# Optimization experiments

Hardware: AMD Instinct MI355X
Metric: run time of the kernel (lower is better)

Reference implementation:

```python
import jax, jax.numpy as jnp
from jax import lax
import numpy as np

N_QUBITS = 10  # min(dim, n_wires) wires carry RX gates; rest stay |0>


def setup_inputs() -> dict:
    key = jax.random.key(0)
    k1, k2, k3, k4 = jax.random.split(key, 4)
    T, B, D, H, C = 128, 512, 512, 512, 32
    inputs = jax.random.normal(k1, (T, B, D), dtype=jnp.float32)
    # 4 gates (f, i, g, o), centres init ~ 0.1 * randn as in the module
    centres = 0.1 * jax.random.normal(k2, (4, C, D + H), dtype=jnp.float32)
    lin_w = jax.random.normal(k3, (4, H, C), dtype=jnp.float32) / jnp.sqrt(jnp.float32(C))
    lin_b = jax.random.normal(k4, (4, H), dtype=jnp.float32) * 0.01
    return {"inputs": inputs, "centres": centres, "lin_w": lin_w, "lin_b": lin_b}


def _quantum_kernel(comb, ctr):
    # comb: [B, dim], ctr: [C, dim]
    # Circuit = RX(x_i) then RX(-y_i) on wire i (i < N_QUBITS) => RX(x_i - y_i).
    # |<0..0|state>| = prod_i |cos((x_i - y_i)/2)| over active wires.
    m = min(comb.shape[-1], N_QUBITS)
    diff = comb[:, None, :m] - ctr[None, :, :m]  # [B, C, m]
    return jnp.prod(jnp.abs(jnp.cos(0.5 * diff)), axis=-1)  # [B, C]


def reference(inputs, centres, lin_w, lin_b):
    T, B, D = inputs.shape
    H = lin_w.shape[1]
    h0 = jnp.zeros((B, H), dtype=inputs.dtype)
    c0 = jnp.zeros((B, H), dtype=inputs.dtype)

    def step(carry, x):
        h, c = carry
        comb = jnp.concatenate([x, h], axis=1)  # [B, D+H]
        # kernels for all 4 gates at once: [4, B, C]
        k = jax.vmap(lambda ct: _quantum_kernel(comb, ct))(centres)
        pre = jnp.einsum('gbc,ghc->gbh', k, lin_w) + lin_b[:, None, :]  # [4, B, H]
        f = jax.nn.sigmoid(pre[0])
        i = jax.nn.sigmoid(pre[1])
        g = jnp.tanh(pre[2])
        o = jax.nn.sigmoid(pre[3])
        c_new = f * c + i * g
        h_new = o * jnp.tanh(c_new)
        return (h_new, c_new), h_new

    (h, c), outputs = lax.scan(step, (h0, c0), inputs)
    return outputs, h, c
```

## Files before the change

kernel.cpp:

```cpp
#include <hip/hip_runtime.h>

#define TT 128
#define BB 512
#define DD 512
#define HH 512
#define CC 32
#define NQ 10
#define GC 128
#define DH 1024
#define CHUNK 8
#define NCHUNK (TT / CHUNK)
#define HLOC 256
#define L2E 1.4426950408889634f

typedef __fp16 h2 __attribute__((ext_vector_type(2)));
typedef __fp16 h4 __attribute__((ext_vector_type(4)));
typedef __fp16 h8 __attribute__((ext_vector_type(8)));
typedef float f4 __attribute__((ext_vector_type(4)));

__device__ __forceinline__ float rcpf(float x) { return __builtin_amdgcn_rcpf(x); }
__device__ __forceinline__ float exp2fast(float x) {
#if __has_builtin(__builtin_amdgcn_exp2f)
    return __builtin_amdgcn_exp2f(x);
#else
    return exp2f(x);
#endif
}

__global__ __launch_bounds__(256, 3) void qlstm_kernel(
    const float* __restrict__ inputs,
    const float* __restrict__ centres,
    const float* __restrict__ lin_w,
    const float* __restrict__ lin_b,
    float* __restrict__ out)
{
    __shared__ __fp16 Klds[TT * GC];
    __shared__ __align__(16) unsigned preBx[CHUNK * HLOC * 2];
    __shared__ float blds[4 * HLOC];

    float* csT = (float*)preBx;
    float* xsA = (float*)preBx + NQ * 128;

    const int bid = blockIdx.x;
    const int b = bid >> 1;
    const int hbase = (bid & 1) * HLOC;

    const int tid = threadIdx.x;
    const int lane = tid & 63;
    const int w = tid >> 6;
    const int q = lane >> 4;
    const int c16 = lane & 15;
    const int hi = lane >> 5;

    for (int idx = tid; idx < TT * NQ; idx += 256) {
        int t = idx / NQ, d = idx - t * NQ;
        xsA[t * 12 + d] = 0.5f * inputs[((size_t)t * BB + b) * DD + d];
    }
    for (int idx = tid; idx < GC * NQ; idx += 256) {
        int gc = idx & 127, d = idx >> 7;
        csT[d * 128 + gc] = 0.5f * centres[(size_t)gc * DH + d];
    }
    for (int idx = tid; idx < 4 * HLOC; idx += 256) {
        int g = idx >> 8, hl = idx & 255;
        float s = (g == 2) ? (2.f * L2E) : (-L2E);
        blds[idx] = s * lin_b[g * HH + hbase + hl];
    }
    __syncthreads();

    h8 bfr[16];
    {
        const int c0 = q * 8;
        #pragma unroll
        for (int g = 0; g < 4; ++g) {
            const float s = (g == 2) ? (2.f * L2E) : (-L2E);
            #pragma unroll
            for (int j = 0; j < 4; ++j) {
                const int hcolg = hbase + w * 64 + j * 16 + c16;
                const float* wp = lin_w + (((size_t)g * HH + hcolg) * CC + c0);
                f4 lo = *(const f4*)wp;
                f4 hif = *(const f4*)(wp + 4);
                h2 p0 = __builtin_amdgcn_cvt_pkrtz(s * lo.x, s * lo.y);
                h2 p1 = __builtin_amdgcn_cvt_pkrtz(s * lo.z, s * lo.w);
                h2 p2 = __builtin_amdgcn_cvt_pkrtz(s * hif.x, s * hif.y);
                h2 p3 = __builtin_amdgcn_cvt_pkrtz(s * hif.z, s * hif.w);
                h8 bb = { p0.x, p0.y, p1.x, p1.y, p2.x, p2.y, p3.x, p3.y };
                bfr[g * 4 + j] = bb;
            }
        }
    }

    {
        const int gcq = (tid & 31) * 4;
        const int t0 = tid >> 5;
        #pragma unroll
        for (int p = 0; p < 16; ++p) {
            const int t = t0 + p * 8;
            float pr0 = 1.f, pr1 = 1.f, pr2 = 1.f, pr3 = 1.f;
            #pragma unroll
            for (int d = 0; d < NQ; ++d) {
                float xd = xsA[t * 12 + d];
                f4 cd = *(const f4*)&csT[d * 128 + gcq];
                pr0 *= fabsf(__cosf(xd - cd.x));
                pr1 *= fabsf(__cosf(xd - cd.y));
                pr2 *= fabsf(__cosf(xd - cd.z));
                pr3 *= fabsf(__cosf(xd - cd.w));
            }
            h2 lo2 = __builtin_amdgcn_cvt_pkrtz(pr0, pr1);
            h2 hi2 = __builtin_amdgcn_cvt_pkrtz(pr2, pr3);
            h4 kk = { lo2.x, lo2.y, hi2.x, hi2.y };
            int byteo = (t * 256 + gcq * 2) ^ ((t & 7) << 4);
            *(h4*)((char*)Klds + byteo) = kk;
        }
    }
    __syncthreads();

    float cs2 = 0.f, hstate = 0.f;
    float* op = out + (size_t)b * HH + hbase + tid;
    const int tlo = c16 & 7;
    int aoff[4];
    #pragma unroll
    for (int g = 0; g < 4; ++g)
        aoff[g] = tlo * 256 + ((g * 64 + q * 16) ^ (tlo << 4));
    const int hclbase = w * 64 + c16;
    const int rl0 = (q & 1) * 4;

    for (int ct = 0; ct < NCHUNK; ++ct) {
        const char* arp = (const char*)Klds + ct * 2048;
        h8 afr[4];
        #pragma unroll
        for (int g = 0; g < 4; ++g)
            afr[g] = *(const h8*)(arp + aoff[g]);

        #pragma unroll
        for (int j = 0; j < 4; ++j) {
            const int hcl = hclbase + j * 16;
            const float bf = blds[0 * HLOC + hcl];
            const float bi = blds[1 * HLOC + hcl];
            const float bg = blds[2 * HLOC + hcl];
            const float bo = blds[3 * HLOC + hcl];
            f4 cf = { bf, bf, bf, bf };
            f4 ci = { bi, bi, bi, bi };
            f4 cg = { bg, bg, bg, bg };
            f4 co = { bo, bo, bo, bo };
            f4 aF = __builtin_amdgcn_mfma_f32_16x16x32_f16(afr[0], bfr[0*4+j], cf, 0, 0, 0);
            f4 aI = __builtin_amdgcn_mfma_f32_16x16x32_f16(afr[1], bfr[1*4+j], ci, 0, 0, 0);
            f4 aG = __builtin_amdgcn_mfma_f32_16x16x32_f16(afr[2], bfr[2*4+j], cg, 0, 0, 0);
            f4 aO = __builtin_amdgcn_mfma_f32_16x16x32_f16(afr[3], bfr[3*4+j], co, 0, 0, 0);
            #pragma unroll
            for (int r = 0; r < 4; ++r) {
                float selA = hi ? aI[r] : aF[r];
                float selB = hi ? aG[r] : aO[r];
                float e1 = rcpf(1.f + exp2fast(selA));
                float e2 = rcpf(1.f + exp2fast(selB));
                float gg2 = fmaf(-4.f * L2E, e2, 2.f * L2E);
                float ig2 = e1 * gg2;
                h2 pk = __builtin_amdgcn_cvt_pkrtz(e1, e2);
                unsigned uval = hi ? __builtin_bit_cast(unsigned, ig2)
                                   : *(unsigned*)&pk;
                preBx[((rl0 + r) * HLOC + hcl) * 2 + hi] = uval;
            }
        }

        #pragma unroll
        for (int s = 0; s < CHUNK; ++s) {
            uint2 vv = *(const uint2*)&preBx[(s * HLOC + tid) * 2];
            h2 fo = *(h2*)&vv.x;
            float F = (float)fo.x;
            float O = (float)fo.y;
            float IG2 = __builtin_bit_cast(float, vv.y);
            cs2 = fmaf(F, cs2, IG2);
            float th = fmaf(-2.f, rcpf(1.f + exp2fast(cs2)), 1.f);
            hstate = O * th;
            op[(size_t)(ct * CHUNK + s) * (BB * HH)] = hstate;
        }
    }

    float* hout = out + (size_t)TT * BB * HH;
    float* cout = hout + (size_t)BB * HH;
    hout[(size_t)b * HH + hbase + tid] = hstate;
    cout[(size_t)b * HH + hbase + tid] = cs2 * 0.34657359027997264f;
}

extern "C" void kernel_launch(void* const* d_in, const int* in_sizes, int n_in,
                              void* d_out, int out_size, void* d_ws, size_t ws_size,
                              hipStream_t stream) {
    const float* inputs  = (const float*)d_in[0];
    const float* centres = (const float*)d_in[1];
    const float* lin_w   = (const float*)d_in[2];
    const float* lin_b   = (const float*)d_in[3];
    float* out = (float*)d_out;

    qlstm_kernel<<<dim3(BB * 2), dim3(256), 0, stream>>>(inputs, centres, lin_w, lin_b, out);
}
```

Baseline: 93.99 us.

## Split quantum-kernel precompute into separate kernel to avoid duplicate computation per batch

Moves the cosine-product quantum kernel computation into its own kernel that writes fp16 kernel values (already swizzled) to a workspace buffer. The main LSTM kernel then just copies them into LDS. Previously both blocks of each batch computed the full 128x128 table, so this work was done twice. The cost is an extra launch plus a 16 MB global round trip. When the workspace is too small, the buffer falls back to a region of the output that is later overwritten, which relies on stream ordering.

New measurement: 99.20 us. 5.5% more time.

```diff
diff --git a/kernel.cpp b/kernel.cpp
--- a/kernel.cpp
+++ b/kernel.cpp
@@ -12,6 +12,7 @@
 #define NCHUNK (TT / CHUNK)
 #define HLOC 256
 #define L2E 1.4426950408889634f
+#define KB_PER_B 32768
 
 typedef __fp16 h2 __attribute__((ext_vector_type(2)));
 typedef __fp16 h4 __attribute__((ext_vector_type(4)));
@@ -27,9 +28,55 @@
 #endif
 }
 
-__global__ __launch_bounds__(256, 3) void qlstm_kernel(
+__global__ __launch_bounds__(256) void qk_kernel(
     const float* __restrict__ inputs,
     const float* __restrict__ centres,
+    __fp16* __restrict__ kbuf)
+{
+    __shared__ float xsA[64 * 12];
+    __shared__ float csT[NQ * 128];
+
+    const int bid = blockIdx.x;
+    const int b = bid >> 1, th = bid & 1;
+    const int tid = threadIdx.x;
+
+    for (int idx = tid; idx < 64 * NQ; idx += 256) {
+        int tl = idx / NQ, d = idx - tl * NQ;
+        xsA[tl * 12 + d] = 0.5f * inputs[((size_t)(th * 64 + tl) * BB + b) * DD + d];
+    }
+    for (int idx = tid; idx < GC * NQ; idx += 256) {
+        int gc = idx & 127, d = idx >> 7;
+        csT[d * 128 + gc] = 0.5f * centres[(size_t)gc * DH + d];
+    }
+    __syncthreads();
+
+    const int gcq = (tid & 31) * 4;
+    const int t0 = tid >> 5;
+    char* kb = (char*)kbuf + (size_t)b * KB_PER_B;
+    #pragma unroll
+    for (int p = 0; p < 8; ++p) {
+        const int tl = t0 + p * 8;
+        const int t = th * 64 + tl;
+        float pr0 = 1.f, pr1 = 1.f, pr2 = 1.f, pr3 = 1.f;
+        #pragma unroll
+        for (int d = 0; d < NQ; ++d) {
+            float xd = xsA[tl * 12 + d];
+            f4 cd = *(const f4*)&csT[d * 128 + gcq];
+            pr0 *= fabsf(__cosf(xd - cd.x));
+            pr1 *= fabsf(__cosf(xd - cd.y));
+            pr2 *= fabsf(__cosf(xd - cd.z));
+            pr3 *= fabsf(__cosf(xd - cd.w));
+        }
+        h2 lo2 = __builtin_amdgcn_cvt_pkrtz(pr0, pr1);
+        h2 hi2 = __builtin_amdgcn_cvt_pkrtz(pr2, pr3);
+        h4 kk = { lo2.x, lo2.y, hi2.x, hi2.y };
+        int byteo = (t * 256 + gcq * 2) ^ ((t & 7) << 4);
+        *(h4*)(kb + byteo) = kk;
+    }
+}
+
+__global__ __launch_bounds__(256, 3) void lstm_kernel(
+    const __fp16* __restrict__ kbuf,
     const float* __restrict__ lin_w,
     const float* __restrict__ lin_b,
     float* __restrict__ out)
@@ -38,9 +85,6 @@
     __shared__ __align__(16) unsigned preBx[CHUNK * HLOC * 2];
     __shared__ float blds[4 * HLOC];
 
-    float* csT = (float*)preBx;
-    float* xsA = (float*)preBx + NQ * 128;
-
     const int bid = blockIdx.x;
     const int b = bid >> 1;
     const int hbase = (bid & 1) * HLOC;
@@ -52,20 +96,26 @@
     const int c16 = lane & 15;
     const int hi = lane >> 5;
 
-    for (int idx = tid; idx < TT * NQ; idx += 256) {
-        int t = idx / NQ, d = idx - t * NQ;
-        xsA[t * 12 + d] = 0.5f * inputs[((size_t)t * BB + b) * DD + d];
-    }
-    for (int idx = tid; idx < GC * NQ; idx += 256) {
-        int gc = idx & 127, d = idx >> 7;
-        csT[d * 128 + gc] = 0.5f * centres[(size_t)gc * DH + d];
-    }
+    {
+        const char* src = (const char*)kbuf + (size_t)b * KB_PER_B;
+        #pragma unroll
+        for (int half = 0; half < 2; ++half) {
+            uint4 t0_ = *(const uint4*)(src + (((half * 4 + 0) * 256 + tid) * 16));
+            uint4 t1_ = *(const uint4*)(src + (((half * 4 + 1) * 256 + tid) * 16));
+            uint4 t2_ = *(const uint4*)(src + (((half * 4 + 2) * 256 + tid) * 16));
+            uint4 t3_ = *(const uint4*)(src + (((half * 4 + 3) * 256 + tid) * 16));
+            *(uint4*)((char*)Klds + (((half * 4 + 0) * 256 + tid) * 16)) = t0_;
+            *(uint4*)((char*)Klds + (((half * 4 + 1) * 256 + tid) * 16)) = t1_;
+            *(uint4*)((char*)Klds + (((half * 4 + 2) * 256 + tid) * 16)) = t2_;
+            *(uint4*)((char*)Klds + (((half * 4 + 3) * 256 + tid) * 16)) = t3_;
+        }
+    }
+
     for (int idx = tid; idx < 4 * HLOC; idx += 256) {
         int g = idx >> 8, hl = idx & 255;
         float s = (g == 2) ? (2.f * L2E) : (-L2E);
         blds[idx] = s * lin_b[g * HH + hbase + hl];
     }
-    __syncthreads();
 
     h8 bfr[16];
     {
@@ -86,30 +136,6 @@
                 h8 bb = { p0.x, p0.y, p1.x, p1.y, p2.x, p2.y, p3.x, p3.y };
                 bfr[g * 4 + j] = bb;
             }
-        }
-    }
-
-    {
-        const int gcq = (tid & 31) * 4;
-        const int t0 = tid >> 5;
-        #pragma unroll
-        for (int p = 0; p < 16; ++p) {
-            const int t = t0 + p * 8;
-            float pr0 = 1.f, pr1 = 1.f, pr2 = 1.f, pr3 = 1.f;
-            #pragma unroll
-            for (int d = 0; d < NQ; ++d) {
-                float xd = xsA[t * 12 + d];
-                f4 cd = *(const f4*)&csT[d * 128 + gcq];
-                pr0 *= fabsf(__cosf(xd - cd.x));
-                pr1 *= fabsf(__cosf(xd - cd.y));
-                pr2 *= fabsf(__cosf(xd - cd.z));
-                pr3 *= fabsf(__cosf(xd - cd.w));
-            }
-            h2 lo2 = __builtin_amdgcn_cvt_pkrtz(pr0, pr1);
-            h2 hi2 = __builtin_amdgcn_cvt_pkrtz(pr2, pr3);
-            h4 kk = { lo2.x, lo2.y, hi2.x, hi2.y };
-            int byteo = (t * 256 + gcq * 2) ^ ((t & 7) << 4);
-            *(h4*)((char*)Klds + byteo) = kk;
         }
     }
     __syncthreads();
@@ -190,5 +216,11 @@
     const float* lin_b   = (const float*)d_in[3];
     float* out = (float*)d_out;
 
-    qlstm_kernel<<<dim3(BB * 2), dim3(256), 0, stream>>>(inputs, centres, lin_w, lin_b, out);
-}
+    const size_t KBYTES = (size_t)BB * KB_PER_B;
+    void* kbuf = (ws_size >= KBYTES)
+               ? d_ws
+               : (void*)((char*)d_out + (size_t)112 * BB * HH * sizeof(float));
+
+    qk_kernel<<<dim3(1024), dim3(256), 0, stream>>>(inputs, centres, (__fp16*)kbuf);
+    lstm_kernel<<<dim3(1024), dim3(256), 0, stream>>>((const __fp16*)kbuf, lin_w, lin_b, out);
+}
```
